# Performance work log

Measured on AMD Instinct MI355X. Metric: run time of the kernel, lower is better.

Reference implementation:

```python
import jax, jax.numpy as jnp
import numpy as np

SPC = 8                                   # samples_per_class
SIG_TEMP = 0.01                           # sigmoid_temperature
K_VALS = (1.0, 2.0, 4.0, 8.0, 16.0)       # all <= batch_size so min(batch,k)=k
K_TEMPS = (1.0, 2.0, 4.0, 8.0, 16.0)


def _sig(x, temp):
    # faithful to original: clamp exponent to [-50, 50]
    e = jnp.clip(-x / temp, -50.0, 50.0)
    return 1.0 / (1.0 + jnp.exp(e))


def setup_inputs() -> dict:
    key = jax.random.key(0)
    preds = jax.random.normal(key, (2048, 1024), dtype=jnp.float32)
    # embeddings are typically L2-normalized before this loss
    preds = preds / jnp.linalg.norm(preds, axis=1, keepdims=True)
    return {"preds": preds, "q_idx": 0}


def reference(preds, q_idx):
    B = preds.shape[0]
    spc = SPC
    kv = jnp.asarray(K_VALS, preds.dtype)          # [K]
    kt = jnp.asarray(K_TEMPS, preds.dtype)         # [K]
    norm_vals = jnp.minimum(kv, float(spc - 1))    # [K]

    idx = jnp.arange(B)
    g = idx // spc            # group id of each query
    r = idx % spc             # position of query within its group

    # all pairwise similarities: S[q, j] = <preds[q], preds[j]>
    S = preds @ preds.T                                        # [B, B]

    # G[q, i] = sim of query q with i-th member of q's own group
    cols = g[:, None] * spc + jnp.arange(spc)[None, :]         # [B, spc]
    G = jnp.take_along_axis(S, cols, axis=1)                   # [B, spc]

    # sim_diff_all[q, j, i] = S[q, j] - G[q, i]
    sg = _sig(S[:, :, None] - G[:, None, :], SIG_TEMP)         # [B, B, spc]

    # zero sim_sg[q, g(q)*spc + i, i]
    jr = jnp.arange(B)[None, :, None]
    ir = jnp.arange(spc)[None, None, :]
    diag_mask = jr == (g[:, None, None] * spc + ir)            # [B, B, spc]
    sg = jnp.where(diag_mask, 0.0, sg)

    # surrogate rank of each in-group sample w.r.t. query q
    rk = 1.0 + sg.sum(axis=1)                                  # [B, spc]
    self_mask = jnp.arange(spc)[None, :] == r[:, None]         # [B, spc]
    rk = jnp.where(self_mask, 0.0, rk)

    # per-k sigmoid indicator rank <= k
    v = _sig(kv[None, None, :] - rk[:, :, None], kt[None, None, :])  # [B, spc, K]
    v = jnp.where(self_mask[:, :, None], 0.0, v)

    recall = jnp.minimum(v.sum(axis=1), kv[None, :]) / norm_vals[None, :]  # [B, K]
    recall_q = recall.mean(axis=1)                                         # [B]
    return jnp.mean(1.0 - recall_q)
```

## Files before the change

kernel.cpp:

```cpp
#include <hip/hip_runtime.h>

#define BATCH 2048
#define DIM   1024
#define SPC   8
#define BM    64
#define BN    64
#define BK    32
#define NKT   (DIM / BK)
#define NJB   (BATCH / BN)

typedef _Float16 half8  __attribute__((ext_vector_type(8)));
typedef _Float16 half4v __attribute__((ext_vector_type(4)));
typedef float    f32x4  __attribute__((ext_vector_type(4)));

constexpr float INV_T    = 1.0f / 0.01f;
constexpr float LO_SCALE = 2048.0f;
constexpr float INV_LO   = 1.0f / 2048.0f;

__device__ __forceinline__ float sig_fast(float x) {
  float e = fminf(fmaxf(-x * INV_T, -50.0f), 50.0f);
  return __builtin_amdgcn_rcpf(1.0f + __expf(e));
}

__device__ __forceinline__ void gl_lds16(const _Float16* g, _Float16* l) {
  __builtin_amdgcn_global_load_lds((const __attribute__((address_space(1))) void*)g,
                                   (__attribute__((address_space(3))) void*)l, 16, 0, 0);
}

__device__ __forceinline__ int swz(int row, int c) { return row * 4 + (c ^ ((row >> 1) & 3)); }

__global__ __launch_bounds__(256) void k_prep(const float* __restrict__ preds,
                                              _Float16* __restrict__ Ph,
                                              _Float16* __restrict__ Pl,
                                              float* __restrict__ G) {
  __shared__ float rows[SPC][DIM + 4];
  __shared__ float part[64][4];
  if (blockIdx.x < BATCH) {
    const int i = blockIdx.x * 256 + threadIdx.x;
    const float4 x = ((const float4*)preds)[i];
    half4v h, l;
    h[0] = (_Float16)x.x; l[0] = (_Float16)((x.x - (float)h[0]) * LO_SCALE);
    h[1] = (_Float16)x.y; l[1] = (_Float16)((x.y - (float)h[1]) * LO_SCALE);
    h[2] = (_Float16)x.z; l[2] = (_Float16)((x.z - (float)h[2]) * LO_SCALE);
    h[3] = (_Float16)x.w; l[3] = (_Float16)((x.w - (float)h[3]) * LO_SCALE);
    ((half4v*)Ph)[i] = h;
    ((half4v*)Pl)[i] = l;
    return;
  }
  const int g = blockIdx.x - BATCH;
  const int tid = threadIdx.x;
  const float4* src = (const float4*)(preds + (size_t)g * SPC * DIM);
#pragma unroll
  for (int c = 0; c < 8; ++c) {
    int idx = c * 256 + tid;
    float4 v = src[idx];
    *(float4*)&rows[idx >> 8][(idx & 255) << 2] = v;
  }
  __syncthreads();
  const int p  = tid & 63;
  const int sl = tid >> 6;
  const float4* ra = (const float4*)&rows[p >> 3][sl * 256];
  const float4* rb = (const float4*)&rows[p & 7][sl * 256];
  float s = 0.0f;
#pragma unroll 8
  for (int e = 0; e < 64; ++e) {
    float4 a = ra[e], b = rb[e];
    s += a.x * b.x + a.y * b.y + a.z * b.z + a.w * b.w;
  }
  part[p][sl] = s;
  __syncthreads();
  if (tid < 64) {
    float v = part[tid][0] + part[tid][1] + part[tid][2] + part[tid][3];
    G[(size_t)(g * SPC + (tid >> 3)) * SPC + (tid & 7)] = v;
  }
}

__global__ __launch_bounds__(256, 4) void k_main(const _Float16* __restrict__ Ph,
                                                 const _Float16* __restrict__ Pl,
                                                 const float* __restrict__ G,
                                                 float* __restrict__ partial) {
  __shared__ __align__(16) _Float16 sAh0[BM * BK], sAl0[BM * BK], sBh0[BN * BK], sBl0[BN * BK];
  __shared__ __align__(16) _Float16 sAh1[BM * BK], sAl1[BM * BK], sBh1[BN * BK], sBl1[BN * BK];
  __shared__ float sRed[2][BM][SPC];
  const int t    = threadIdx.x;
  const int lane = t & 63;
  const int w    = t >> 6;
  const int wr   = w >> 1, wc = w & 1;

  const int d    = blockIdx.y * 32 + blockIdx.x;
  const int xcd  = d & 7, idx = d >> 3;
  const int jbIdx = xcd * 4 + (idx & 3);
  const int qb    = (idx >> 2) * BM;
  const int jb    = jbIdx * BN;

  f32x4 accH[2][2], accX[2][2];
#pragma unroll
  for (int m = 0; m < 2; ++m)
#pragma unroll
    for (int n = 0; n < 2; ++n) {
      accH[m][n] = (f32x4){0.f, 0.f, 0.f, 0.f};
      accX[m][n] = (f32x4){0.f, 0.f, 0.f, 0.f};
    }

  auto STAGE = [&](_Float16* dAh, _Float16* dAl, _Float16* dBh, _Float16* dBl, int kt) {
    const int kk  = kt * BK;
    const int row = t >> 2;
    const int c   = (t & 3) ^ ((row >> 1) & 3);
    const size_t sA = (size_t)(qb + row) * DIM + kk + c * 8;
    const size_t sB = (size_t)(jb + row) * DIM + kk + c * 8;
    gl_lds16(Ph + sA, dAh + (size_t)t * 8);
    gl_lds16(Pl + sA, dAl + (size_t)t * 8);
    gl_lds16(Ph + sB, dBh + (size_t)t * 8);
    gl_lds16(Pl + sB, dBl + (size_t)t * 8);
  };

  const int rl = lane & 15, ch = lane >> 4;
  auto COMPUTE = [&](const _Float16* bAh, const _Float16* bAl,
                     const _Float16* bBh, const _Float16* bBl) {
    half8 ah[2], al[2], bh[2], bl[2];
#pragma unroll
    for (int m = 0; m < 2; ++m) {
      const int s = swz(wr * 32 + m * 16 + rl, ch);
      ah[m] = *(const half8*)&bAh[(size_t)s * 8];
      al[m] = *(const half8*)&bAl[(size_t)s * 8];
    }
#pragma unroll
    for (int n = 0; n < 2; ++n) {
      const int s = swz(wc * 32 + n * 16 + rl, ch);
      bh[n] = *(const half8*)&bBh[(size_t)s * 8];
      bl[n] = *(const half8*)&bBl[(size_t)s * 8];
    }
#pragma unroll
    for (int m = 0; m < 2; ++m)
#pragma unroll
      for (int n = 0; n < 2; ++n) {
        accH[m][n] = __builtin_amdgcn_mfma_f32_16x16x32_f16(ah[m], bh[n], accH[m][n], 0, 0, 0);
        accX[m][n] = __builtin_amdgcn_mfma_f32_16x16x32_f16(ah[m], bl[n], accX[m][n], 0, 0, 0);
        accX[m][n] = __builtin_amdgcn_mfma_f32_16x16x32_f16(al[m], bh[n], accX[m][n], 0, 0, 0);
      }
  };

  STAGE(sAh0, sAl0, sBh0, sBl0, 0);
  __syncthreads();
#pragma unroll 1
  for (int kt = 0; kt < NKT; kt += 2) {
    if (kt + 1 < NKT) STAGE(sAh1, sAl1, sBh1, sBl1, kt + 1);
    COMPUTE(sAh0, sAl0, sBh0, sBl0);
    __syncthreads();
    if (kt + 2 < NKT) STAGE(sAh0, sAl0, sBh0, sBl0, kt + 2);
    COMPUTE(sAh1, sAl1, sBh1, sBl1);
    __syncthreads();
  }

  const int colLane = lane & 15;
  const int rowLane = lane >> 4;
#pragma unroll
  for (int m = 0; m < 2; ++m) {
#pragma unroll
    for (int v = 0; v < 4; ++v) {
      const int ql = wr * 32 + m * 16 + rowLane * 4 + v;
      const int q  = qb + ql;
      const float4 g0 = *(const float4*)&G[(size_t)q * 8];
      const float4 g1 = *(const float4*)&G[(size_t)q * 8 + 4];
      const float gv[8] = {g0.x, g0.y, g0.z, g0.w, g1.x, g1.y, g1.z, g1.w};
      const int qg = q >> 3;
      float sv[2];
      int jg[2], jp[2];
#pragma unroll
      for (int n = 0; n < 2; ++n) {
        sv[n] = accH[m][n][v] + accX[m][n][v] * INV_LO;
        const int j = jb + wc * 32 + n * 16 + colLane;
        jg[n] = j >> 3;
        jp[n] = j & 7;
      }
#pragma unroll
      for (int i = 0; i < 8; ++i) {
        float pr = 0.0f;
#pragma unroll
        for (int n = 0; n < 2; ++n) {
          float s = sig_fast(sv[n] - gv[i]);
          if (jg[n] == qg && jp[n] == i) s = 0.0f;
          pr += s;
        }
        pr += __shfl_xor(pr, 1);
        pr += __shfl_xor(pr, 2);
        pr += __shfl_xor(pr, 4);
        pr += __shfl_xor(pr, 8);
        if (colLane == 0) sRed[wc][ql][i] = pr;
      }
    }
  }
  __syncthreads();
  if (t < 128) {
    const float* r0 = &sRed[0][0][0];
    const float* r1 = &sRed[1][0][0];
    float4 a = *(const float4*)&r0[t * 4];
    float4 b = *(const float4*)&r1[t * 4];
    float4 s = {a.x + b.x, a.y + b.y, a.z + b.z, a.w + b.w};
    *(float4*)&partial[((size_t)jbIdx * BATCH + qb) * SPC + t * 4] = s;
  }
}

__global__ __launch_bounds__(256) void k_fin(const float* __restrict__ partial,
                                             float* __restrict__ out) {
  const int tg = blockIdx.x * 256 + threadIdx.x;
  const int q = tg >> 3, i = tg & 7;
  float rk = 1.0f;
#pragma unroll 8
  for (int p = 0; p < NJB; ++p)
    rk += partial[(size_t)p * BATCH * SPC + tg];
  const float kv[5]  = {1.f, 2.f, 4.f, 8.f, 16.f};
  const float rkt[5] = {1.f, 0.5f, 0.25f, 0.125f, 0.0625f};
  const float nv[5]  = {1.f, 2.f, 4.f, 7.f, 7.f};
  const bool self = (i == (q & 7));
  float vs[5];
#pragma unroll
  for (int k = 0; k < 5; ++k) {
    float e = (rk - kv[k]) * rkt[k];
    e = fminf(fmaxf(e, -50.0f), 50.0f);
    float v = 1.0f / (1.0f + __expf(e));
    vs[k] = self ? 0.0f : v;
  }
#pragma unroll
  for (int o = 1; o < 8; o <<= 1)
#pragma unroll
    for (int k = 0; k < 5; ++k) vs[k] += __shfl_xor(vs[k], o);
  float tv = 0.0f;
  if (i == 0) {
    float rq = 0.0f;
#pragma unroll
    for (int k = 0; k < 5; ++k) rq += fminf(vs[k], kv[k]) / nv[k];
    tv = (1.0f - rq * 0.2f) * (1.0f / (float)BATCH);
  }
#pragma unroll
  for (int o = 1; o < 64; o <<= 1) tv += __shfl_xor(tv, o);
  __shared__ float sw[4];
  if ((threadIdx.x & 63) == 0) sw[threadIdx.x >> 6] = tv;
  __syncthreads();
  if (threadIdx.x == 0) atomicAdd(out, sw[0] + sw[1] + sw[2] + sw[3]);
}

extern "C" void kernel_launch(void* const* d_in, const int* in_sizes, int n_in,
                              void* d_out, int out_size, void* d_ws, size_t ws_size,
                              hipStream_t stream) {
  const float* preds = (const float*)d_in[0];
  float* G       = (float*)d_ws;
  float* partial = (float*)((char*)d_ws + (64 << 10));
  _Float16* Ph   = (_Float16*)((char*)d_ws + (64 << 10) + (2 << 20));
  _Float16* Pl   = Ph + (size_t)BATCH * DIM;
  hipMemsetAsync(d_out, 0, sizeof(float), stream);
  k_prep<<<BATCH + BATCH / SPC, 256, 0, stream>>>(preds, Ph, Pl, G);
  k_main<<<dim3(32, 32), 256, 0, stream>>>(Ph, Pl, G, partial);
  k_fin<<<64, 256, 0, stream>>>(partial, (float*)d_out);
}
```

Before: 121.6 us.

## Restructure into GEMM writing S matrix and a separate per-query loss kernel

Drops the prep kernel by loading fp32 preds directly in the GEMM and splitting them into hi/lo fp16 in registers before writing to LDS. The similarity tile is written to a full BxB S matrix in global memory, fp32 or fp16 depending on workspace size. A separate loss kernel then computes the sigmoid ranks per query row, reading the in-group similarities from S. This also removes the memset and the finish kernel, since block 0 zeroes the output. In exchange it adds global traffic for S and redoes the fp32-to-fp16 split on every tile load instead of once.

```diff
diff --git a/kernel.cpp b/kernel.cpp
--- a/kernel.cpp
+++ b/kernel.cpp
@@ -7,11 +7,9 @@
 #define BN    64
 #define BK    32
 #define NKT   (DIM / BK)
-#define NJB   (BATCH / BN)
-
-typedef _Float16 half8  __attribute__((ext_vector_type(8)));
-typedef _Float16 half4v __attribute__((ext_vector_type(4)));
-typedef float    f32x4  __attribute__((ext_vector_type(4)));
+
+typedef _Float16 half8 __attribute__((ext_vector_type(8)));
+typedef float    f32x4 __attribute__((ext_vector_type(4)));
 
 constexpr float INV_T    = 1.0f / 0.01f;
 constexpr float LO_SCALE = 2048.0f;
@@ -22,76 +20,33 @@
   return __builtin_amdgcn_rcpf(1.0f + __expf(e));
 }
 
-__device__ __forceinline__ void gl_lds16(const _Float16* g, _Float16* l) {
-  __builtin_amdgcn_global_load_lds((const __attribute__((address_space(1))) void*)g,
-                                   (__attribute__((address_space(3))) void*)l, 16, 0, 0);
-}
-
 __device__ __forceinline__ int swz(int row, int c) { return row * 4 + (c ^ ((row >> 1) & 3)); }
 
-__global__ __launch_bounds__(256) void k_prep(const float* __restrict__ preds,
-                                              _Float16* __restrict__ Ph,
-                                              _Float16* __restrict__ Pl,
-                                              float* __restrict__ G) {
-  __shared__ float rows[SPC][DIM + 4];
-  __shared__ float part[64][4];
-  if (blockIdx.x < BATCH) {
-    const int i = blockIdx.x * 256 + threadIdx.x;
-    const float4 x = ((const float4*)preds)[i];
-    half4v h, l;
-    h[0] = (_Float16)x.x; l[0] = (_Float16)((x.x - (float)h[0]) * LO_SCALE);
-    h[1] = (_Float16)x.y; l[1] = (_Float16)((x.y - (float)h[1]) * LO_SCALE);
-    h[2] = (_Float16)x.z; l[2] = (_Float16)((x.z - (float)h[2]) * LO_SCALE);
-    h[3] = (_Float16)x.w; l[3] = (_Float16)((x.w - (float)h[3]) * LO_SCALE);
-    ((half4v*)Ph)[i] = h;
-    ((half4v*)Pl)[i] = l;
-    return;
-  }
-  const int g = blockIdx.x - BATCH;
-  const int tid = threadIdx.x;
-  const float4* src = (const float4*)(preds + (size_t)g * SPC * DIM);
-#pragma unroll
-  for (int c = 0; c < 8; ++c) {
-    int idx = c * 256 + tid;
-    float4 v = src[idx];
-    *(float4*)&rows[idx >> 8][(idx & 255) << 2] = v;
-  }
-  __syncthreads();
-  const int p  = tid & 63;
-  const int sl = tid >> 6;
-  const float4* ra = (const float4*)&rows[p >> 3][sl * 256];
-  const float4* rb = (const float4*)&rows[p & 7][sl * 256];
-  float s = 0.0f;
-#pragma unroll 8
-  for (int e = 0; e < 64; ++e) {
-    float4 a = ra[e], b = rb[e];
-    s += a.x * b.x + a.y * b.y + a.z * b.z + a.w * b.w;
-  }
-  part[p][sl] = s;
-  __syncthreads();
-  if (tid < 64) {
-    float v = part[tid][0] + part[tid][1] + part[tid][2] + part[tid][3];
-    G[(size_t)(g * SPC + (tid >> 3)) * SPC + (tid & 7)] = v;
-  }
-}
-
-__global__ __launch_bounds__(256, 4) void k_main(const _Float16* __restrict__ Ph,
-                                                 const _Float16* __restrict__ Pl,
-                                                 const float* __restrict__ G,
-                                                 float* __restrict__ partial) {
-  __shared__ __align__(16) _Float16 sAh0[BM * BK], sAl0[BM * BK], sBh0[BN * BK], sBl0[BN * BK];
-  __shared__ __align__(16) _Float16 sAh1[BM * BK], sAl1[BM * BK], sBh1[BN * BK], sBl1[BN * BK];
-  __shared__ float sRed[2][BM][SPC];
+template <bool S16>
+__global__ __launch_bounds__(256, 4) void k_gemm(const float* __restrict__ P,
+                                                 void* __restrict__ Sout,
+                                                 float* __restrict__ out0) {
+  __shared__ __align__(16) char LDSBUF[32768];
+  _Float16* sAh0 = (_Float16*)(LDSBUF);
+  _Float16* sAl0 = (_Float16*)(LDSBUF + 4096);
+  _Float16* sBh0 = (_Float16*)(LDSBUF + 8192);
+  _Float16* sBl0 = (_Float16*)(LDSBUF + 12288);
+  _Float16* sAh1 = (_Float16*)(LDSBUF + 16384);
+  _Float16* sAl1 = (_Float16*)(LDSBUF + 20480);
+  _Float16* sBh1 = (_Float16*)(LDSBUF + 24576);
+  _Float16* sBl1 = (_Float16*)(LDSBUF + 28672);
+
   const int t    = threadIdx.x;
   const int lane = t & 63;
   const int w    = t >> 6;
   const int wr   = w >> 1, wc = w & 1;
 
-  const int d    = blockIdx.y * 32 + blockIdx.x;
-  const int xcd  = d & 7, idx = d >> 3;
+  const int d = blockIdx.y * 32 + blockIdx.x;
+  if (d == 0 && t == 0) *out0 = 0.0f;
+  const int xcd = d & 7, idx = d >> 3;
   const int jbIdx = xcd * 4 + (idx & 3);
-  const int qb    = (idx >> 2) * BM;
-  const int jb    = jbIdx * BN;
+  const int qb = (idx >> 2) * BM;
+  const int jb = jbIdx * BN;
 
   f32x4 accH[2][2], accX[2][2];
 #pragma unroll
@@ -102,16 +57,39 @@
       accX[m][n] = (f32x4){0.f, 0.f, 0.f, 0.f};
     }
 
-  auto STAGE = [&](_Float16* dAh, _Float16* dAl, _Float16* dBh, _Float16* dBl, int kt) {
-    const int kk  = kt * BK;
-    const int row = t >> 2;
-    const int c   = (t & 3) ^ ((row >> 1) & 3);
-    const size_t sA = (size_t)(qb + row) * DIM + kk + c * 8;
-    const size_t sB = (size_t)(jb + row) * DIM + kk + c * 8;
-    gl_lds16(Ph + sA, dAh + (size_t)t * 8);
-    gl_lds16(Pl + sA, dAl + (size_t)t * 8);
-    gl_lds16(Ph + sB, dBh + (size_t)t * 8);
-    gl_lds16(Pl + sB, dBl + (size_t)t * 8);
+  const int srow  = t >> 2;
+  const int sc    = t & 3;
+  const int wslot = swz(srow, sc);
+
+  f32x4 rA0, rA1, rB0, rB1;
+  auto LOADREGS = [&](int kt) {
+    const float* pa = P + (size_t)(qb + srow) * DIM + kt * BK + sc * 8;
+    const float* pb = P + (size_t)(jb + srow) * DIM + kt * BK + sc * 8;
+    rA0 = *(const f32x4*)pa; rA1 = *(const f32x4*)(pa + 4);
+    rB0 = *(const f32x4*)pb; rB1 = *(const f32x4*)(pb + 4);
+  };
+  auto SPLITW = [&](_Float16* dAh, _Float16* dAl, _Float16* dBh, _Float16* dBl) {
+    half8 h, l;
+    {
+      float xs[8] = {rA0[0], rA0[1], rA0[2], rA0[3], rA1[0], rA1[1], rA1[2], rA1[3]};
+#pragma unroll
+      for (int e = 0; e < 8; ++e) {
+        h[e] = (_Float16)xs[e];
+        l[e] = (_Float16)((xs[e] - (float)h[e]) * LO_SCALE);
+      }
+      *(half8*)&dAh[wslot * 8] = h;
+      *(half8*)&dAl[wslot * 8] = l;
+    }
+    {
+      float xs[8] = {rB0[0], rB0[1], rB0[2], rB0[3], rB1[0], rB1[1], rB1[2], rB1[3]};
+#pragma unroll
+      for (int e = 0; e < 8; ++e) {
+        h[e] = (_Float16)xs[e];
+        l[e] = (_Float16)((xs[e] - (float)h[e]) * LO_SCALE);
+      }
+      *(half8*)&dBh[wslot * 8] = h;
+      *(half8*)&dBl[wslot * 8] = l;
+    }
   };
 
   const int rl = lane & 15, ch = lane >> 4;
@@ -140,102 +118,116 @@
       }
   };
 
-  STAGE(sAh0, sAl0, sBh0, sBl0, 0);
+  LOADREGS(0);
+  SPLITW(sAh0, sAl0, sBh0, sBl0);
+  LOADREGS(1);
   __syncthreads();
 #pragma unroll 1
   for (int kt = 0; kt < NKT; kt += 2) {
-    if (kt + 1 < NKT) STAGE(sAh1, sAl1, sBh1, sBl1, kt + 1);
     COMPUTE(sAh0, sAl0, sBh0, sBl0);
+    SPLITW(sAh1, sAl1, sBh1, sBl1);
+    if (kt + 2 < NKT) LOADREGS(kt + 2);
     __syncthreads();
-    if (kt + 2 < NKT) STAGE(sAh0, sAl0, sBh0, sBl0, kt + 2);
     COMPUTE(sAh1, sAl1, sBh1, sBl1);
+    if (kt + 2 < NKT) {
+      SPLITW(sAh0, sAl0, sBh0, sBl0);
+      if (kt + 3 < NKT) LOADREGS(kt + 3);
+    }
     __syncthreads();
   }
 
-  const int colLane = lane & 15;
-  const int rowLane = lane >> 4;
-#pragma unroll
-  for (int m = 0; m < 2; ++m) {
-#pragma unroll
-    for (int v = 0; v < 4; ++v) {
-      const int ql = wr * 32 + m * 16 + rowLane * 4 + v;
-      const int q  = qb + ql;
-      const float4 g0 = *(const float4*)&G[(size_t)q * 8];
-      const float4 g1 = *(const float4*)&G[(size_t)q * 8 + 4];
-      const float gv[8] = {g0.x, g0.y, g0.z, g0.w, g1.x, g1.y, g1.z, g1.w};
-      const int qg = q >> 3;
-      float sv[2];
-      int jg[2], jp[2];
-#pragma unroll
-      for (int n = 0; n < 2; ++n) {
-        sv[n] = accH[m][n][v] + accX[m][n][v] * INV_LO;
-        const int j = jb + wc * 32 + n * 16 + colLane;
-        jg[n] = j >> 3;
-        jp[n] = j & 7;
-      }
+  float* stile = (float*)LDSBUF;
+  const int colL = lane & 15, rowL = lane >> 4;
+#pragma unroll
+  for (int m = 0; m < 2; ++m)
+#pragma unroll
+    for (int n = 0; n < 2; ++n)
+#pragma unroll
+      for (int v = 0; v < 4; ++v) {
+        const int r = wr * 32 + m * 16 + rowL * 4 + v;
+        const int c = wc * 32 + n * 16 + colL;
+        stile[r * 68 + c] = accH[m][n][v] + accX[m][n][v] * INV_LO;
+      }
+  __syncthreads();
+  {
+    const int row = t >> 2, c4 = t & 3;
+    const float* src = &stile[row * 68 + c4 * 16];
+    if (S16) {
+      _Float16* S = (_Float16*)Sout + (size_t)(qb + row) * BATCH + jb + c4 * 16;
+      half8 h0, h1;
+#pragma unroll
+      for (int e = 0; e < 8; ++e) { h0[e] = (_Float16)src[e]; h1[e] = (_Float16)src[8 + e]; }
+      *(half8*)S = h0;
+      *(half8*)(S + 8) = h1;
+    } else {
+      float* S = (float*)Sout + (size_t)(qb + row) * BATCH + jb + c4 * 16;
+      f32x4 v0 = *(const f32x4*)(src);
+      f32x4 v1 = *(const f32x4*)(src + 4);
+      f32x4 v2 = *(const f32x4*)(src + 8);
+      f32x4 v3 = *(const f32x4*)(src + 12);
+      *(f32x4*)(S)      = v0;
+      *(f32x4*)(S + 4)  = v1;
+      *(f32x4*)(S + 8)  = v2;
+      *(f32x4*)(S + 12) = v3;
+    }
+  }
+}
+
+template <bool S16>
+__global__ __launch_bounds__(256) void k_loss(const void* __restrict__ Sv,
+                                              float* __restrict__ out) {
+  const int w = threadIdx.x >> 6, lane = threadIdx.x & 63;
+  const int q = blockIdx.x * 4 + w;
+  const int qg = q >> 3;
+  const float* Sf = (const float*)Sv;
+  const _Float16* Sh = (const _Float16*)Sv;
+
+  float gv[8];
+#pragma unroll
+  for (int i = 0; i < 8; ++i)
+    gv[i] = S16 ? (float)Sh[(size_t)q * BATCH + qg * 8 + i]
+                : Sf[(size_t)q * BATCH + qg * 8 + i];
+
+  float acc[8] = {0.f, 0.f, 0.f, 0.f, 0.f, 0.f, 0.f, 0.f};
+#pragma unroll 4
+  for (int jj = 0; jj < 32; ++jj) {
+    const int j = jj * 64 + lane;
+    const float s = S16 ? (float)Sh[(size_t)q * BATCH + j] : Sf[(size_t)q * BATCH + j];
+    const int ex = ((j >> 3) == qg) ? (j & 7) : -1;
+#pragma unroll
+    for (int i = 0; i < 8; ++i) {
+      float v = sig_fast(s - gv[i]);
+      acc[i] += (i == ex) ? 0.0f : v;
+    }
+  }
+#pragma unroll
+  for (int o = 1; o < 64; o <<= 1)
+#pragma unroll
+    for (int i = 0; i < 8; ++i) acc[i] += __shfl_xor(acc[i], o);
+
+  float tv = 0.0f;
+  if (lane == 0) {
+    const float kv[5]  = {1.f, 2.f, 4.f, 8.f, 16.f};
+    const float rkt[5] = {1.f, 0.5f, 0.25f, 0.125f, 0.0625f};
+    const float nv[5]  = {1.f, 2.f, 4.f, 7.f, 7.f};
+    const int r = q & 7;
+    float rq = 0.0f;
+#pragma unroll
+    for (int k = 0; k < 5; ++k) {
+      float vs = 0.0f;
 #pragma unroll
       for (int i = 0; i < 8; ++i) {
-        float pr = 0.0f;
-#pragma unroll
-        for (int n = 0; n < 2; ++n) {
-          float s = sig_fast(sv[n] - gv[i]);
-          if (jg[n] == qg && jp[n] == i) s = 0.0f;
-          pr += s;
-        }
-        pr += __shfl_xor(pr, 1);
-        pr += __shfl_xor(pr, 2);
-        pr += __shfl_xor(pr, 4);
-        pr += __shfl_xor(pr, 8);
-        if (colLane == 0) sRed[wc][ql][i] = pr;
-      }
-    }
-  }
-  __syncthreads();
-  if (t < 128) {
-    const float* r0 = &sRed[0][0][0];
-    const float* r1 = &sRed[1][0][0];
-    float4 a = *(const float4*)&r0[t * 4];
-    float4 b = *(const float4*)&r1[t * 4];
-    float4 s = {a.x + b.x, a.y + b.y, a.z + b.z, a.w + b.w};
-    *(float4*)&partial[((size_t)jbIdx * BATCH + qb) * SPC + t * 4] = s;
-  }
-}
-
-__global__ __launch_bounds__(256) void k_fin(const float* __restrict__ partial,
-                                             float* __restrict__ out) {
-  const int tg = blockIdx.x * 256 + threadIdx.x;
-  const int q = tg >> 3, i = tg & 7;
-  float rk = 1.0f;
-#pragma unroll 8
-  for (int p = 0; p < NJB; ++p)
-    rk += partial[(size_t)p * BATCH * SPC + tg];
-  const float kv[5]  = {1.f, 2.f, 4.f, 8.f, 16.f};
-  const float rkt[5] = {1.f, 0.5f, 0.25f, 0.125f, 0.0625f};
-  const float nv[5]  = {1.f, 2.f, 4.f, 7.f, 7.f};
-  const bool self = (i == (q & 7));
-  float vs[5];
-#pragma unroll
-  for (int k = 0; k < 5; ++k) {
-    float e = (rk - kv[k]) * rkt[k];
-    e = fminf(fmaxf(e, -50.0f), 50.0f);
-    float v = 1.0f / (1.0f + __expf(e));
-    vs[k] = self ? 0.0f : v;
-  }
-#pragma unroll
-  for (int o = 1; o < 8; o <<= 1)
-#pragma unroll
-    for (int k = 0; k < 5; ++k) vs[k] += __shfl_xor(vs[k], o);
-  float tv = 0.0f;
-  if (i == 0) {
-    float rq = 0.0f;
-#pragma unroll
-    for (int k = 0; k < 5; ++k) rq += fminf(vs[k], kv[k]) / nv[k];
+        const float rk = 1.0f + acc[i];
+        float e = fminf(fmaxf((rk - kv[k]) * rkt[k], -50.0f), 50.0f);
+        float v = 1.0f / (1.0f + __expf(e));
+        vs += (i == r) ? 0.0f : v;
+      }
+      rq += fminf(vs, kv[k]) / nv[k];
+    }
     tv = (1.0f - rq * 0.2f) * (1.0f / (float)BATCH);
   }
-#pragma unroll
-  for (int o = 1; o < 64; o <<= 1) tv += __shfl_xor(tv, o);
   __shared__ float sw[4];
-  if ((threadIdx.x & 63) == 0) sw[threadIdx.x >> 6] = tv;
+  if (lane == 0) sw[w] = tv;
   __syncthreads();
   if (threadIdx.x == 0) atomicAdd(out, sw[0] + sw[1] + sw[2] + sw[3]);
 }
@@ -244,12 +236,12 @@
                               void* d_out, int out_size, void* d_ws, size_t ws_size,
                               hipStream_t stream) {
   const float* preds = (const float*)d_in[0];
-  float* G       = (float*)d_ws;
-  float* partial = (float*)((char*)d_ws + (64 << 10));
-  _Float16* Ph   = (_Float16*)((char*)d_ws + (64 << 10) + (2 << 20));
-  _Float16* Pl   = Ph + (size_t)BATCH * DIM;
-  hipMemsetAsync(d_out, 0, sizeof(float), stream);
-  k_prep<<<BATCH + BATCH / SPC, 256, 0, stream>>>(preds, Ph, Pl, G);
-  k_main<<<dim3(32, 32), 256, 0, stream>>>(Ph, Pl, G, partial);
-  k_fin<<<64, 256, 0, stream>>>(partial, (float*)d_out);
-}
+  float* out = (float*)d_out;
+  if (ws_size >= (size_t)BATCH * BATCH * sizeof(float)) {
+    k_gemm<false><<<dim3(32, 32), 256, 0, stream>>>(preds, d_ws, out);
+    k_loss<false><<<BATCH / 4, 256, 0, stream>>>(d_ws, out);
+  } else {
+    k_gemm<true><<<dim3(32, 32), 256, 0, stream>>>(preds, d_ws, out);
+    k_loss<true><<<BATCH / 4, 256, 0, stream>>>(d_ws, out);
+  }
+}
```

After: 119.4 us. About the same (-1.8%).
